# Optimization experiments

Measured on AMD Instinct MI355X. Metric: run time of the kernel, lower is better.

## Reference

```python
import jax, jax.numpy as jnp
import numpy as np

B, N, L, H = 8, 2048, 1280, 160
GAMMA = 1.0  # fixed buffer, gamma_init_value=1, not trainable


def setup_inputs() -> dict:
    key = jax.random.key(0)
    ks = jax.random.split(key, 7)
    s_in = 1.0 / np.sqrt(L)  # conv1d default init scale (approx; randn used for testing)
    return {
        "x": jax.random.normal(ks[0], (B, N, L), dtype=jnp.float32),
        "Wq": jax.random.normal(ks[1], (H, L), dtype=jnp.float32) * s_in,
        "bq": jax.random.normal(ks[2], (H,), dtype=jnp.float32) * s_in,
        "Wk": jax.random.normal(ks[3], (H, L), dtype=jnp.float32) * s_in,
        "bk": jax.random.normal(ks[4], (H,), dtype=jnp.float32) * s_in,
        "Wv": jax.random.normal(ks[5], (L, L), dtype=jnp.float32) * s_in,
        "bv": jax.random.normal(ks[6], (L,), dtype=jnp.float32) * s_in,
    }


def reference(x, Wq, bq, Wk, bk, Wv, bv):
    # 1x1 Conv1d on x.permute(0,2,1) == per-token linear projection
    q = jnp.einsum("bnl,hl->bnh", x, Wq) + bq          # [B,N,H]
    k = jnp.einsum("bnl,hl->bnh", x, Wk) + bk          # [B,N,H]
    v = jnp.einsum("bnl,ml->bnm", x, Wv) + bv          # [B,N,L]
    energy = jnp.einsum("bih,bjh->bij", q, k)          # [B,N,N]
    attn = jax.nn.softmax(energy, axis=-1)
    out = jnp.einsum("bij,bjm->bim", attn, v)          # [B,N,L]
    return GAMMA * out + x                              # [B,N,L]
```

## Files before the change

kernel.cpp:

```cpp
#include <hip/hip_runtime.h>

#define BB 8
#define NN 2048
#define LL 1280
#define HH 160
#define BN (BB*NN)
#define NO (2*HH + LL)
#define SHIFT 40.0f

typedef __attribute__((ext_vector_type(8))) short short8;
typedef __attribute__((ext_vector_type(4))) float floatx4;

__device__ __forceinline__ unsigned short f2bf(float f) {
    unsigned int u = __builtin_bit_cast(unsigned int, f);
    u = (u + 0x7FFFu + ((u >> 16) & 1u)) >> 16;
    return (unsigned short)u;
}
__device__ __forceinline__ float bf2f(unsigned short h) {
    unsigned int u = ((unsigned int)h) << 16;
    return __builtin_bit_cast(float, u);
}
__device__ __forceinline__ void split2(float f, unsigned short& hi, unsigned short& lo) {
    hi = f2bf(f);
    lo = f2bf(f - bf2f(hi));
}


__global__ __launch_bounds__(256) void cast_w(
    const float* __restrict__ Wq, const float* __restrict__ Wk, const float* __restrict__ Wv,
    unsigned short* __restrict__ wqk_h, unsigned short* __restrict__ wqk_l,
    unsigned short* __restrict__ wv)
{
    int o = blockIdx.x;
    if (o < 2*HH) {
        const float* src = (o < HH) ? (Wq + (size_t)o * LL) : (Wk + (size_t)(o - HH) * LL);
        unsigned short* dh = wqk_h + (size_t)o * LL;
        unsigned short* dl = wqk_l + (size_t)o * LL;
        for (int c = threadIdx.x; c < LL; c += 256) {
            unsigned short h, l;
            split2(src[c], h, l);
            dh[c] = h; dl[c] = l;
        }
    } else {
        const float* src = Wv + (size_t)(o - 2*HH) * LL;
        unsigned short* dst = wv + (size_t)(o - 2*HH) * LL;
        for (int c = threadIdx.x * 4; c < LL; c += 256 * 4) {
            float4 f = *(const float4*)(src + c);
            ushort4 u;
            u.x = f2bf(f.x); u.y = f2bf(f.y); u.z = f2bf(f.z); u.w = f2bf(f.w);
            *(ushort4*)(dst + c) = u;
        }
    }
}

__global__ __launch_bounds__(256, 2) void proj_qk(
    const float* __restrict__ x,
    const unsigned short* __restrict__ wh, const unsigned short* __restrict__ wl,
    const float* __restrict__ bq, const float* __restrict__ bk,
    unsigned short* __restrict__ qh, unsigned short* __restrict__ ql,
    unsigned short* __restrict__ kh, unsigned short* __restrict__ kl)
{
    __shared__ __align__(16) unsigned short Ah[128 * 40];
    __shared__ __align__(16) unsigned short Al[128 * 40];
    __shared__ __align__(16) unsigned short Bh[64 * 40];
    __shared__ __align__(16) unsigned short Bl[64 * 40];

    const int o0 = blockIdx.x * 64;
    const int m0 = blockIdx.y * 128;
    const int tid = threadIdx.x;
    const int wave = tid >> 6, lane = tid & 63;
    const int l15 = lane & 15, l4 = lane >> 4;

    floatx4 acc[2][4] = {};

    const int sr = tid >> 2;
    const int sc = (tid & 3) * 8;

    for (int k0 = 0; k0 < LL; k0 += 32) {
        __syncthreads();
        #pragma unroll
        for (int h = 0; h < 2; h++) {
            int r = sr + h * 64;
            const float* xp = x + (size_t)(m0 + r) * LL + k0 + sc;
            float4 f0 = *(const float4*)xp;
            float4 f1 = *(const float4*)(xp + 4);
            float fv[8] = {f0.x, f0.y, f0.z, f0.w, f1.x, f1.y, f1.z, f1.w};
            short8 h8, l8;
            #pragma unroll
            for (int i = 0; i < 8; i++) {
                unsigned short hh, lll;
                split2(fv[i], hh, lll);
                h8[i] = (short)hh; l8[i] = (short)lll;
            }
            *(short8*)&Ah[r * 40 + sc] = h8;
            *(short8*)&Al[r * 40 + sc] = l8;
        }
        *(short8*)&Bh[sr * 40 + sc] = *(const short8*)&wh[(size_t)(o0 + sr) * LL + k0 + sc];
        *(short8*)&Bl[sr * 40 + sc] = *(const short8*)&wl[(size_t)(o0 + sr) * LL + k0 + sc];
        __syncthreads();

        short8 ah0 = *(const short8*)&Ah[(wave * 32 + l15) * 40 + l4 * 8];
        short8 ah1 = *(const short8*)&Ah[(wave * 32 + 16 + l15) * 40 + l4 * 8];
        short8 al0 = *(const short8*)&Al[(wave * 32 + l15) * 40 + l4 * 8];
        short8 al1 = *(const short8*)&Al[(wave * 32 + 16 + l15) * 40 + l4 * 8];
        #pragma unroll
        for (int ct = 0; ct < 4; ct++) {
            short8 bh8 = *(const short8*)&Bh[(ct * 16 + l15) * 40 + l4 * 8];
            short8 bl8 = *(const short8*)&Bl[(ct * 16 + l15) * 40 + l4 * 8];
            acc[0][ct] = __builtin_amdgcn_mfma_f32_16x16x32_bf16(ah0, bh8, acc[0][ct], 0, 0, 0);
            acc[0][ct] = __builtin_amdgcn_mfma_f32_16x16x32_bf16(al0, bh8, acc[0][ct], 0, 0, 0);
            acc[0][ct] = __builtin_amdgcn_mfma_f32_16x16x32_bf16(ah0, bl8, acc[0][ct], 0, 0, 0);
            acc[1][ct] = __builtin_amdgcn_mfma_f32_16x16x32_bf16(ah1, bh8, acc[1][ct], 0, 0, 0);
            acc[1][ct] = __builtin_amdgcn_mfma_f32_16x16x32_bf16(al1, bh8, acc[1][ct], 0, 0, 0);
            acc[1][ct] = __builtin_amdgcn_mfma_f32_16x16x32_bf16(ah1, bl8, acc[1][ct], 0, 0, 0);
        }
    }

    #pragma unroll
    for (int rt = 0; rt < 2; rt++)
        #pragma unroll
        for (int ct = 0; ct < 4; ct++)
            #pragma unroll
            for (int r = 0; r < 4; r++) {
                int m = m0 + wave * 32 + rt * 16 + l4 * 4 + r;
                int o = o0 + ct * 16 + l15;
                float val = acc[rt][ct][r] + ((o < HH) ? bq[o] : bk[o - HH]);
                unsigned short vh, vl;
                split2(val, vh, vl);
                int oo = (o < HH) ? o : (o - HH);
                size_t fa = (size_t)(m >> 4) * 2560 + (oo >> 5) * 512
                          + ((oo >> 3) & 3) * 128 + (m & 15) * 8 + (oo & 7);
                if (o < HH) {
                    qh[fa] = vh;
                    ql[fa] = vl;
                } else {
                    kh[fa] = vh;
                    kl[fa] = vl;
                }
            }
}

__global__ __launch_bounds__(256, 2) void proj_v(
    const float* __restrict__ x, const unsigned short* __restrict__ wv,
    const float* __restrict__ bv, unsigned short* __restrict__ vt)
{
    __shared__ __align__(16) unsigned char smem[128 * 136 * 2];
    unsigned short* As = (unsigned short*)smem;
    unsigned short* Bs = As + 128 * 40;

    const int o0 = blockIdx.x * 128;
    const int m0 = blockIdx.y * 128;
    const int tid = threadIdx.x;
    const int wave = tid >> 6, lane = tid & 63;
    const int l15 = lane & 15, l4 = lane >> 4;

    floatx4 acc[2][8] = {};

    const int sr = tid >> 2;
    const int sc = (tid & 3) * 8;

    for (int k0 = 0; k0 < LL; k0 += 32) {
        __syncthreads();
        #pragma unroll
        for (int h = 0; h < 2; h++) {
            int r = sr + h * 64;
            const float* xp = x + (size_t)(m0 + r) * LL + k0 + sc;
            float4 f0 = *(const float4*)xp;
            float4 f1 = *(const float4*)(xp + 4);
            short8 h8;
            h8[0]=(short)f2bf(f0.x); h8[1]=(short)f2bf(f0.y); h8[2]=(short)f2bf(f0.z); h8[3]=(short)f2bf(f0.w);
            h8[4]=(short)f2bf(f1.x); h8[5]=(short)f2bf(f1.y); h8[6]=(short)f2bf(f1.z); h8[7]=(short)f2bf(f1.w);
            *(short8*)&As[r * 40 + sc] = h8;
            *(short8*)&Bs[r * 40 + sc] =
                *(const short8*)&wv[(size_t)(o0 + r) * LL + k0 + sc];
        }
        __syncthreads();
        short8 af0 = *(const short8*)&As[(wave * 32 + l15) * 40 + l4 * 8];
        short8 af1 = *(const short8*)&As[(wave * 32 + 16 + l15) * 40 + l4 * 8];
        #pragma unroll
        for (int ct = 0; ct < 8; ct++) {
            short8 bf = *(const short8*)&Bs[(ct * 16 + l15) * 40 + l4 * 8];
            acc[0][ct] = __builtin_amdgcn_mfma_f32_16x16x32_bf16(af0, bf, acc[0][ct], 0, 0, 0);
            acc[1][ct] = __builtin_amdgcn_mfma_f32_16x16x32_bf16(af1, bf, acc[1][ct], 0, 0, 0);
        }
    }

    __syncthreads();
    unsigned short* trs = (unsigned short*)smem;

    #pragma unroll
    for (int rt = 0; rt < 2; rt++)
        #pragma unroll
        for (int ct = 0; ct < 8; ct++)
            #pragma unroll
            for (int r = 0; r < 4; r++) {
                int ml = wave * 32 + rt * 16 + l4 * 4 + r;
                int cl = ct * 16 + l15;
                trs[cl * 136 + ml] = f2bf(acc[rt][ct][r] + bv[o0 + cl]);
            }
    __syncthreads();
    {
        int bidx = m0 >> 11;
        int nb0 = m0 & 2047;
        int cl = tid >> 1;
        int f = o0 + cl;
        const unsigned short* srcr = trs + cl * 136 + (tid & 1) * 64;
        unsigned short* dstF = vt + (size_t)bidx * LL * NN
                             + (size_t)(f >> 4) * 32768 + (f & 15) * 8;
        int nb = nb0 + (tid & 1) * 64;
        #pragma unroll
        for (int i = 0; i < 8; i++) {
            int n = nb + i * 8;
            *(short8*)(dstF + (size_t)(n >> 5) * 512 + ((n >> 3) & 3) * 128)
                = *(const short8*)(srcr + i * 8);
        }
    }
}

__global__ __launch_bounds__(256, 2) void s_exp(
    const unsigned short* __restrict__ qhp, const unsigned short* __restrict__ qlp,
    const unsigned short* __restrict__ khp, const unsigned short* __restrict__ klp,
    unsigned short* __restrict__ P, float* __restrict__ Lsum)
{
    __shared__ float sums[4][32];
    const int b  = blockIdx.y;
    const int i0 = blockIdx.x * 32;
    const int tid = threadIdx.x;
    const int wave = tid >> 6, lane = tid & 63;
    const int l15 = lane & 15, l4 = lane >> 4;

    short8 aqh[2][5], aql[2][5];
    #pragma unroll
    for (int rt = 0; rt < 2; rt++) {
        const size_t rowb = (size_t)((b * NN + i0 + rt * 16) >> 4) * 2560 + lane * 8;
        #pragma unroll
        for (int ks = 0; ks < 5; ks++) {
            aqh[rt][ks] = *(const short8*)&qhp[rowb + ks * 512];
            aql[rt][ks] = *(const short8*)&qlp[rowb + ks * 512];
        }
    }

    float sr[2][4] = {};
    unsigned short* Pb = P + (size_t)b * NN * NN + (size_t)(i0 >> 4) * 32768;

    for (int c0 = 0; c0 < NN; c0 += 256) {
        const int jb = c0 + wave * 64;
        #pragma unroll
        for (int ct = 0; ct < 4; ct++) {
            const int tok0 = jb + ct * 16;
            const int tok  = tok0 + l15;
            const size_t kbase = (size_t)((b * NN + tok0) >> 4) * 2560 + lane * 8;
            floatx4 a0[3] = {{0,0,0,0},{0,0,0,0},{0,0,0,0}};
            floatx4 a1[3] = {{0,0,0,0},{0,0,0,0},{0,0,0,0}};
            #pragma unroll
            for (int ks = 0; ks < 5; ks++) {
                short8 bh = *(const short8*)&khp[kbase + ks * 512];
                short8 bl = *(const short8*)&klp[kbase + ks * 512];
                a0[0] = __builtin_amdgcn_mfma_f32_16x16x32_bf16(aqh[0][ks], bh, a0[0], 0, 0, 0);
                a0[1] = __builtin_amdgcn_mfma_f32_16x16x32_bf16(aql[0][ks], bh, a0[1], 0, 0, 0);
                a0[2] = __builtin_amdgcn_mfma_f32_16x16x32_bf16(aqh[0][ks], bl, a0[2], 0, 0, 0);
                a1[0] = __builtin_amdgcn_mfma_f32_16x16x32_bf16(aqh[1][ks], bh, a1[0], 0, 0, 0);
                a1[1] = __builtin_amdgcn_mfma_f32_16x16x32_bf16(aql[1][ks], bh, a1[1], 0, 0, 0);
                a1[2] = __builtin_amdgcn_mfma_f32_16x16x32_bf16(aqh[1][ks], bl, a1[2], 0, 0, 0);
            }
            const size_t tbase = (size_t)(tok >> 5) * 512 + ((tok >> 3) & 3) * 128 + (tok & 7);
            #pragma unroll
            for (int r = 0; r < 4; r++) {
                float e0 = a0[0][r] + a0[1][r] + a0[2][r];
                float e1 = a1[0][r] + a1[1][r] + a1[2][r];
                unsigned short pb0 = f2bf(__expf(e0 - SHIFT));
                unsigned short pb1 = f2bf(__expf(e1 - SHIFT));
                Pb[tbase + (l4 * 4 + r) * 8] = pb0;
                Pb[tbase + (l4 * 4 + r) * 8 + 32768] = pb1;
                sr[0][r] += bf2f(pb0);
                sr[1][r] += bf2f(pb1);
            }
        }
    }

    #pragma unroll
    for (int rt = 0; rt < 2; rt++)
        #pragma unroll
        for (int r = 0; r < 4; r++) {
            float v = sr[rt][r];
            v += __shfl_xor(v, 1);
            v += __shfl_xor(v, 2);
            v += __shfl_xor(v, 4);
            v += __shfl_xor(v, 8);
            if (l15 == 0) sums[wave][rt * 16 + l4 * 4 + r] = v;
        }
    __syncthreads();
    if (tid < 32)
        Lsum[(size_t)b * NN + i0 + tid] =
            sums[0][tid] + sums[1][tid] + sums[2][tid] + sums[3][tid];
}

__device__ __forceinline__ void gl16(const unsigned short* g, unsigned short* l) {
    __builtin_amdgcn_global_load_lds(
        (const __attribute__((address_space(1))) unsigned int*)g,
        (__attribute__((address_space(3))) unsigned int*)l, 16, 0, 0);
}

__global__ __launch_bounds__(256, 3) void pv_gemm(
    const unsigned short* __restrict__ P, const unsigned short* __restrict__ vt,
    const float* __restrict__ Lsum,
    const float* __restrict__ x, float* __restrict__ out)
{
    __shared__ __align__(16) unsigned short Sm[3 * 8192];

    const int p0 = blockIdx.x;
    const int b  = p0 & 7;
    const int t  = p0 >> 3;
    const int n0 = (t % 10) * 128;
    const int m0 = (t / 10) * 128;

    const int tid = threadIdx.x;
    const int wave = tid >> 6, lane = tid & 63;
    const int l15 = lane & 15, l4 = lane >> 4;
    const int wm = wave >> 1, wn = wave & 1;

    const unsigned short* PbF = P  + (size_t)b * NN * NN + (size_t)(m0 >> 4) * 32768;
    const unsigned short* VbF = vt + (size_t)b * LL * NN + (size_t)(n0 >> 4) * 32768;

    const int sp0 = tid, sp1 = 256 + tid;
    const unsigned sa0 = (unsigned)(sp0 >> 6) * 32768u + (sp0 & 63) * 8;
    const unsigned sa1 = (unsigned)(sp1 >> 6) * 32768u + (sp1 & 63) * 8;

    floatx4 acc[4][4] = {};

    auto STAGE = [&](int slot, int ks) {
        unsigned short* A  = Sm + slot * 8192;
        unsigned short* Bs = A + 4096;
        const unsigned ko = (unsigned)ks * 512u;
        gl16(PbF + sa0 + ko, A  + sp0 * 8);
        gl16(VbF + sa0 + ko, Bs + sp0 * 8);
        gl16(PbF + sa1 + ko, A  + sp1 * 8);
        gl16(VbF + sa1 + ko, Bs + sp1 * 8);
    };

    auto COMPUTE = [&](int slot) {
        const unsigned short* A  = Sm + slot * 8192;
        const unsigned short* Bs = A + 4096;
        short8 a[4], bb[4];
        #pragma unroll
        for (int mf = 0; mf < 4; mf++)
            a[mf] = *(const short8*)(A + ((wm * 4 + mf) * 64 + lane) * 8);
        #pragma unroll
        for (int nf = 0; nf < 4; nf++)
            bb[nf] = *(const short8*)(Bs + ((wn * 4 + nf) * 64 + lane) * 8);
        __builtin_amdgcn_s_setprio(1);
        #pragma unroll
        for (int mf = 0; mf < 4; mf++)
            #pragma unroll
            for (int nf = 0; nf < 4; nf++)
                acc[mf][nf] = __builtin_amdgcn_mfma_f32_16x16x32_bf16(a[mf], bb[nf], acc[mf][nf], 0, 0, 0);
        __builtin_amdgcn_s_setprio(0);
    };

    STAGE(0, 0); STAGE(1, 1); STAGE(2, 2);

    int s = 0;
    for (int kt = 0; kt < 61; ++kt) {
        asm volatile("s_waitcnt vmcnt(8)" ::: "memory");
        asm volatile("s_barrier" ::: "memory");
        COMPUTE(s);
        asm volatile("s_barrier" ::: "memory");
        STAGE(s, kt + 3);
        s = (s == 2) ? 0 : s + 1;
    }
    asm volatile("s_waitcnt vmcnt(8)" ::: "memory");
    asm volatile("s_barrier" ::: "memory");
    COMPUTE(s); s = (s == 2) ? 0 : s + 1;
    asm volatile("s_waitcnt vmcnt(4)" ::: "memory");
    asm volatile("s_barrier" ::: "memory");
    COMPUTE(s); s = (s == 2) ? 0 : s + 1;
    asm volatile("s_waitcnt vmcnt(0)" ::: "memory");
    asm volatile("s_barrier" ::: "memory");
    COMPUTE(s);

    float linv[4][4];
    #pragma unroll
    for (int mf = 0; mf < 4; mf++)
        #pragma unroll
        for (int r = 0; r < 4; r++)
            linv[mf][r] = 1.0f / Lsum[(size_t)b * NN + m0 + wm * 64 + mf * 16 + l4 * 4 + r];

    #pragma unroll
    for (int mf = 0; mf < 4; mf++)
        #pragma unroll
        for (int nf = 0; nf < 4; nf++)
            #pragma unroll
            for (int r = 0; r < 4; r++) {
                int row = m0 + wm * 64 + mf * 16 + l4 * 4 + r;
                int col = n0 + wn * 64 + nf * 16 + l15;
                size_t idx = ((size_t)b * NN + row) * LL + col;
                out[idx] = acc[mf][nf][r] * linv[mf][r] + x[idx];
            }
}

extern "C" void kernel_launch(void* const* d_in, const int* in_sizes, int n_in,
                              void* d_out, int out_size, void* d_ws, size_t ws_size,
                              hipStream_t stream) {
    const float* x  = (const float*)d_in[0];
    const float* Wq = (const float*)d_in[1];
    const float* bq = (const float*)d_in[2];
    const float* Wk = (const float*)d_in[3];
    const float* bk = (const float*)d_in[4];
    const float* Wv = (const float*)d_in[5];
    const float* bv = (const float*)d_in[6];
    float* out = (float*)d_out;

    unsigned short* wqk_h = (unsigned short*)d_ws;
    unsigned short* wqk_l = wqk_h + (size_t)2*HH * LL;
    unsigned short* wv    = wqk_l + (size_t)2*HH * LL;
    unsigned short* qh    = wv    + (size_t)LL * LL;
    unsigned short* ql    = qh    + (size_t)BN * HH;
    unsigned short* kh    = ql    + (size_t)BN * HH;
    unsigned short* kl    = kh    + (size_t)BN * HH;
    unsigned short* vt    = kl    + (size_t)BN * HH;
    unsigned short* P     = vt    + (size_t)BB * LL * NN;
    float*          Lsum  = (float*)(P + (size_t)BB * NN * NN);

    cast_w<<<dim3(NO), dim3(256), 0, stream>>>(Wq, Wk, Wv, wqk_h, wqk_l, wv);

    dim3 gqk(2*HH / 64, BN / 128);
    proj_qk<<<gqk, dim3(256), 0, stream>>>(x, wqk_h, wqk_l, bq, bk, qh, ql, kh, kl);

    dim3 gv(LL / 128, BN / 128);
    proj_v<<<gv, dim3(256), 0, stream>>>(x, wv, bv, vt);

    dim3 gs(NN / 32, BB);
    s_exp<<<gs, dim3(256), 0, stream>>>(qh, ql, kh, kl, P, Lsum);

    pv_gemm<<<dim3(1280), dim3(256), 0, stream>>>(P, vt, Lsum, x, out);
}
```

Measured before the change: 527.6 us.

## Pre-cast x to bf16 fragment layout and pipeline proj_v with async LDS loads

Adds a cast_x kernel that converts x to bf16 in an MFMA-fragment-friendly tiled layout (stored in the P workspace region), and re-lays the bf16 Wv into the same layout. proj_v is rewritten as a triple-buffered global_load_lds pipeline with 4x4 MFMA tiles per wave, XCD-aware block mapping, and direct fragment-layout stores to vt without an LDS transpose. This removes per-iteration fp32 loads and conversions from the V projection's inner loop. The cost is an extra pass over x and another kernel launch.

```diff
diff --git a/kernel.cpp b/kernel.cpp
--- a/kernel.cpp
+++ b/kernel.cpp
@@ -25,6 +25,12 @@
     lo = f2bf(f - bf2f(hi));
 }
 
+
+__device__ __forceinline__ void gl16(const unsigned short* g, unsigned short* l) {
+    __builtin_amdgcn_global_load_lds(
+        (const __attribute__((address_space(1))) unsigned int*)g,
+        (__attribute__((address_space(3))) unsigned int*)l, 16, 0, 0);
+}
 
 __global__ __launch_bounds__(256) void cast_w(
     const float* __restrict__ Wq, const float* __restrict__ Wk, const float* __restrict__ Wv,
@@ -42,14 +48,35 @@
             dh[c] = h; dl[c] = l;
         }
     } else {
-        const float* src = Wv + (size_t)(o - 2*HH) * LL;
-        unsigned short* dst = wv + (size_t)(o - 2*HH) * LL;
+        int f = o - 2*HH;
+        const float* src = Wv + (size_t)f * LL;
+        unsigned short* dstF = wv + (size_t)(f >> 4) * 20480 + (f & 15) * 8;
         for (int c = threadIdx.x * 4; c < LL; c += 256 * 4) {
-            float4 f = *(const float4*)(src + c);
+            float4 v = *(const float4*)(src + c);
             ushort4 u;
-            u.x = f2bf(f.x); u.y = f2bf(f.y); u.z = f2bf(f.z); u.w = f2bf(f.w);
-            *(ushort4*)(dst + c) = u;
-        }
+            u.x = f2bf(v.x); u.y = f2bf(v.y); u.z = f2bf(v.z); u.w = f2bf(v.w);
+            *(ushort4*)(dstF + (size_t)(c >> 5) * 512 + ((c >> 3) & 3) * 128 + (c & 7)) = u;
+        }
+    }
+}
+
+__global__ __launch_bounds__(256) void cast_x(
+    const float* __restrict__ x, unsigned short* __restrict__ xh)
+{
+    const int g   = blockIdx.x;
+    const int tid = threadIdx.x;
+    const float* src = x + (size_t)(g * 16 + (tid & 15)) * LL + ((tid >> 4) & 3) * 8;
+    unsigned short* dst = xh + (size_t)g * 20480 + tid * 8;
+    const int ks0 = tid >> 6;
+    #pragma unroll
+    for (int it = 0; it < 10; it++) {
+        int k0 = (it * 4 + ks0) * 32;
+        float4 f0 = *(const float4*)(src + k0);
+        float4 f1 = *(const float4*)(src + k0 + 4);
+        short8 h8;
+        h8[0]=(short)f2bf(f0.x); h8[1]=(short)f2bf(f0.y); h8[2]=(short)f2bf(f0.z); h8[3]=(short)f2bf(f0.w);
+        h8[4]=(short)f2bf(f1.x); h8[5]=(short)f2bf(f1.y); h8[6]=(short)f2bf(f1.z); h8[7]=(short)f2bf(f1.w);
+        *(short8*)(dst + it * 2048) = h8;
     }
 }
 
@@ -140,81 +167,106 @@
             }
 }
 
-__global__ __launch_bounds__(256, 2) void proj_v(
-    const float* __restrict__ x, const unsigned short* __restrict__ wv,
+__global__ __launch_bounds__(256, 3) void proj_v(
+    const unsigned short* __restrict__ xh, const unsigned short* __restrict__ wv,
     const float* __restrict__ bv, unsigned short* __restrict__ vt)
 {
-    __shared__ __align__(16) unsigned char smem[128 * 136 * 2];
-    unsigned short* As = (unsigned short*)smem;
-    unsigned short* Bs = As + 128 * 40;
-
-    const int o0 = blockIdx.x * 128;
-    const int m0 = blockIdx.y * 128;
+    __shared__ __align__(16) unsigned short Sm[3 * 8192];
+
+    const int bid = blockIdx.x;
+    const int xcd = bid & 7;
+    const int q   = bid >> 3;
+    const int mt  = xcd * 16 + q / 10;
+    const int ft  = q % 10;
+    const int m0 = mt * 128;
+    const int f0 = ft * 128;
+
     const int tid = threadIdx.x;
     const int wave = tid >> 6, lane = tid & 63;
     const int l15 = lane & 15, l4 = lane >> 4;
-
-    floatx4 acc[2][8] = {};
-
-    const int sr = tid >> 2;
-    const int sc = (tid & 3) * 8;
-
-    for (int k0 = 0; k0 < LL; k0 += 32) {
-        __syncthreads();
-        #pragma unroll
-        for (int h = 0; h < 2; h++) {
-            int r = sr + h * 64;
-            const float* xp = x + (size_t)(m0 + r) * LL + k0 + sc;
-            float4 f0 = *(const float4*)xp;
-            float4 f1 = *(const float4*)(xp + 4);
-            short8 h8;
-            h8[0]=(short)f2bf(f0.x); h8[1]=(short)f2bf(f0.y); h8[2]=(short)f2bf(f0.z); h8[3]=(short)f2bf(f0.w);
-            h8[4]=(short)f2bf(f1.x); h8[5]=(short)f2bf(f1.y); h8[6]=(short)f2bf(f1.z); h8[7]=(short)f2bf(f1.w);
-            *(short8*)&As[r * 40 + sc] = h8;
-            *(short8*)&Bs[r * 40 + sc] =
-                *(const short8*)&wv[(size_t)(o0 + r) * LL + k0 + sc];
-        }
-        __syncthreads();
-        short8 af0 = *(const short8*)&As[(wave * 32 + l15) * 40 + l4 * 8];
-        short8 af1 = *(const short8*)&As[(wave * 32 + 16 + l15) * 40 + l4 * 8];
-        #pragma unroll
-        for (int ct = 0; ct < 8; ct++) {
-            short8 bf = *(const short8*)&Bs[(ct * 16 + l15) * 40 + l4 * 8];
-            acc[0][ct] = __builtin_amdgcn_mfma_f32_16x16x32_bf16(af0, bf, acc[0][ct], 0, 0, 0);
-            acc[1][ct] = __builtin_amdgcn_mfma_f32_16x16x32_bf16(af1, bf, acc[1][ct], 0, 0, 0);
-        }
-    }
-
-    __syncthreads();
-    unsigned short* trs = (unsigned short*)smem;
-
-    #pragma unroll
-    for (int rt = 0; rt < 2; rt++)
-        #pragma unroll
-        for (int ct = 0; ct < 8; ct++)
-            #pragma unroll
-            for (int r = 0; r < 4; r++) {
-                int ml = wave * 32 + rt * 16 + l4 * 4 + r;
-                int cl = ct * 16 + l15;
-                trs[cl * 136 + ml] = f2bf(acc[rt][ct][r] + bv[o0 + cl]);
-            }
-    __syncthreads();
-    {
-        int bidx = m0 >> 11;
-        int nb0 = m0 & 2047;
-        int cl = tid >> 1;
-        int f = o0 + cl;
-        const unsigned short* srcr = trs + cl * 136 + (tid & 1) * 64;
-        unsigned short* dstF = vt + (size_t)bidx * LL * NN
-                             + (size_t)(f >> 4) * 32768 + (f & 15) * 8;
-        int nb = nb0 + (tid & 1) * 64;
-        #pragma unroll
-        for (int i = 0; i < 8; i++) {
-            int n = nb + i * 8;
-            *(short8*)(dstF + (size_t)(n >> 5) * 512 + ((n >> 3) & 3) * 128)
-                = *(const short8*)(srcr + i * 8);
-        }
-    }
+    const int wm = wave >> 1, wn = wave & 1;
+
+    const unsigned short* AF = xh + (size_t)(m0 >> 4) * 20480;
+    const unsigned short* BF = wv + (size_t)(f0 >> 4) * 20480;
+
+    const int sp0 = tid, sp1 = 256 + tid;
+    const unsigned sa0 = (unsigned)(sp0 >> 6) * 20480u + (sp0 & 63) * 8;
+    const unsigned sa1 = (unsigned)(sp1 >> 6) * 20480u + (sp1 & 63) * 8;
+
+    floatx4 acc[4][4] = {};
+
+    auto STAGE = [&](int slot, int ks) {
+        unsigned short* A  = Sm + slot * 8192;
+        unsigned short* Bs = A + 4096;
+        const unsigned ko = (unsigned)ks * 512u;
+        gl16(AF + sa0 + ko, A  + sp0 * 8);
+        gl16(BF + sa0 + ko, Bs + sp0 * 8);
+        gl16(AF + sa1 + ko, A  + sp1 * 8);
+        gl16(BF + sa1 + ko, Bs + sp1 * 8);
+    };
+
+    auto COMPUTE = [&](int slot) {
+        const unsigned short* A  = Sm + slot * 8192;
+        const unsigned short* Bs = A + 4096;
+        short8 a[4], bb[4];
+        #pragma unroll
+        for (int mf = 0; mf < 4; mf++)
+            a[mf] = *(const short8*)(A + ((wm * 4 + mf) * 64 + lane) * 8);
+        #pragma unroll
+        for (int nf = 0; nf < 4; nf++)
+            bb[nf] = *(const short8*)(Bs + ((wn * 4 + nf) * 64 + lane) * 8);
+        __builtin_amdgcn_s_setprio(1);
+        #pragma unroll
+        for (int mf = 0; mf < 4; mf++)
+            #pragma unroll
+            for (int nf = 0; nf < 4; nf++)
+                acc[mf][nf] = __builtin_amdgcn_mfma_f32_16x16x32_bf16(a[mf], bb[nf], acc[mf][nf], 0, 0, 0);
+        __builtin_amdgcn_s_setprio(0);
+    };
+
+    STAGE(0, 0); STAGE(1, 1); STAGE(2, 2);
+
+    int s = 0;
+    for (int kt = 0; kt < 37; ++kt) {
+        asm volatile("s_waitcnt vmcnt(8)" ::: "memory");
+        asm volatile("s_barrier" ::: "memory");
+        COMPUTE(s);
+        asm volatile("s_barrier" ::: "memory");
+        STAGE(s, kt + 3);
+        s = (s == 2) ? 0 : s + 1;
+    }
+    asm volatile("s_waitcnt vmcnt(8)" ::: "memory");
+    asm volatile("s_barrier" ::: "memory");
+    COMPUTE(s); s = (s == 2) ? 0 : s + 1;
+    asm volatile("s_waitcnt vmcnt(4)" ::: "memory");
+    asm volatile("s_barrier" ::: "memory");
+    COMPUTE(s); s = (s == 2) ? 0 : s + 1;
+    asm volatile("s_waitcnt vmcnt(0)" ::: "memory");
+    asm volatile("s_barrier" ::: "memory");
+    COMPUTE(s);
+
+    const int b    = m0 >> 11;
+    const int tokb = (m0 & 2047) + wm * 64;
+    unsigned short* vtB = vt + (size_t)b * LL * NN;
+    float bvv[4];
+    #pragma unroll
+    for (int nf = 0; nf < 4; nf++)
+        bvv[nf] = bv[f0 + wn * 64 + nf * 16 + l15];
+
+    #pragma unroll
+    for (int mf = 0; mf < 4; mf++)
+        #pragma unroll
+        for (int nf = 0; nf < 4; nf++) {
+            int f   = f0 + wn * 64 + nf * 16 + l15;
+            int tok = tokb + mf * 16 + l4 * 4;
+            ushort4 u;
+            u.x = f2bf(acc[mf][nf][0] + bvv[nf]);
+            u.y = f2bf(acc[mf][nf][1] + bvv[nf]);
+            u.z = f2bf(acc[mf][nf][2] + bvv[nf]);
+            u.w = f2bf(acc[mf][nf][3] + bvv[nf]);
+            *(ushort4*)(vtB + (size_t)(f >> 4) * 32768 + (tok >> 5) * 512
+                        + ((tok >> 3) & 3) * 128 + (f & 15) * 8 + (tok & 7)) = u;
+        }
 }
 
 __global__ __launch_bounds__(256, 2) void s_exp(
@@ -295,12 +347,6 @@
             sums[0][tid] + sums[1][tid] + sums[2][tid] + sums[3][tid];
 }
 
-__device__ __forceinline__ void gl16(const unsigned short* g, unsigned short* l) {
-    __builtin_amdgcn_global_load_lds(
-        (const __attribute__((address_space(1))) unsigned int*)g,
-        (__attribute__((address_space(3))) unsigned int*)l, 16, 0, 0);
-}
-
 __global__ __launch_bounds__(256, 3) void pv_gemm(
     const unsigned short* __restrict__ P, const unsigned short* __restrict__ vt,
     const float* __restrict__ Lsum,
@@ -420,14 +466,16 @@
     unsigned short* vt    = kl    + (size_t)BN * HH;
     unsigned short* P     = vt    + (size_t)BB * LL * NN;
     float*          Lsum  = (float*)(P + (size_t)BB * NN * NN);
+    unsigned short* xh    = P;
 
     cast_w<<<dim3(NO), dim3(256), 0, stream>>>(Wq, Wk, Wv, wqk_h, wqk_l, wv);
+
+    cast_x<<<dim3(BN / 16), dim3(256), 0, stream>>>(x, xh);
 
     dim3 gqk(2*HH / 64, BN / 128);
     proj_qk<<<gqk, dim3(256), 0, stream>>>(x, wqk_h, wqk_l, bq, bk, qh, ql, kh, kl);
 
-    dim3 gv(LL / 128, BN / 128);
-    proj_v<<<gv, dim3(256), 0, stream>>>(x, wv, bv, vt);
+    proj_v<<<dim3(1280), dim3(256), 0, stream>>>(xh, wv, bv, vt);
 
     dim3 gs(NN / 32, BB);
     s_exp<<<gs, dim3(256), 0, stream>>>(qh, ql, kh, kl, P, Lsum);
```

Measured after the change: 479.2 us. 1.1x faster.
